# Optimization experiments

Hardware: AMD Instinct MI355X
Metric: run time of the kernel (lower is better)

Reference implementation:

```python
import jax, jax.numpy as jnp
import numpy as np

N, H, HD = 512, 8, 128          # n_nodes, n_heads, h feature dim
M0, M1 = 256, 256               # mlp_units
NORM_CONST = 1.0


def setup_inputs() -> dict:
    key = jax.random.key(0)
    ks = jax.random.split(key, 16)
    def w(k, i, o, scale=1.0):
        return jax.random.normal(k, (i, o), jnp.float32) * (scale / np.sqrt(i))
    F = HD + H * H               # h_concat dim = 128 + 64 = 192
    EIN = H + 2 * F              # edge MLP input dim = 8 + 384 = 392
    return {
        "x": jax.random.normal(ks[0], (N, H, 3), jnp.float32),
        "h": jax.random.normal(ks[1], (N, HD), jnp.float32),
        # phi_e: MLP([256,256], silu, activate_final=True)
        "We0": w(ks[2], EIN, M0), "be0": jnp.zeros((M0,), jnp.float32),
        "We1": w(ks[3], M0, M1), "be1": jnp.zeros((M1,), jnp.float32),
        # phi_inf: Linear(1) + sigmoid
        "Winf": w(ks[4], M1, 1), "binf": jnp.zeros((1,), jnp.float32),
        # phi_x: MLP([256,256], silu, activate_final=True) -> Linear(n_heads) (variance-scaled small init)
        "Wx0": w(ks[5], M1, M0), "bx0": jnp.zeros((M0,), jnp.float32),
        "Wx1": w(ks[6], M0, M1), "bx1": jnp.zeros((M1,), jnp.float32),
        "Wxo": w(ks[7], M1, H, scale=0.03), "bxo": jnp.zeros((H,), jnp.float32),
        # phi_h: MLP([256,256], silu, activate_final=False)... note haiku MLP applies
        # activation between layers; final Linear(h_dim) appended in forward.
        "Wh0": w(ks[8], M1 + HD, M0), "bh0": jnp.zeros((M0,), jnp.float32),
        "Wh1": w(ks[9], M0, M1), "bh1": jnp.zeros((M1,), jnp.float32),
        "Who": w(ks[10], M1, HD), "bho": jnp.zeros((HD,), jnp.float32),
    }


def _forward(x, h, We0, be0, We1, be1, Winf, binf, Wx0, bx0, Wx1, bx1,
             Wxo, bxo, Wh0, bh0, Wh1, bh1, Who, bho):
    n, nh = x.shape[0], x.shape[1]
    silu = jax.nn.silu
    off = 1.0 - jnp.eye(n, dtype=x.dtype)                  # off-diagonal node mask
    # per-node head-pair squared distances -> [N, H*H] (diag naturally 0)
    dh = x[:, :, None, :] - x[:, None, :, :]               # [N,H,H,3]
    sqh = jnp.sum(dh * dh, axis=-1).reshape(n, nh * nh)
    hc = jnp.concatenate([h, sqh], axis=-1)                # [N, F]
    # all-pairs node diffs per head: dn[i,j,h] = x[j,h] - x[i,h]
    dn = x[None] - x[:, None]                              # [N,N,H,3]
    sqn = jnp.sum(dn * dn, axis=-1)                        # [N,N,H]
    F = hc.shape[-1]
    hc_j = jnp.broadcast_to(hc[None], (n, n, F))           # receiver-side: hc[j]
    hc_i = jnp.broadcast_to(hc[:, None], (n, n, F))        # sender-side: hc[i]
    edge_in = jnp.concatenate([sqn, hc_j, hc_i], axis=-1)  # [N,N,H+2F]
    # phi_e (activate_final=True), zero self-edges
    m = silu(silu(edge_in @ We0 + be0) @ We1 + be1) * off[:, :, None]
    # gate + message aggregation
    e = jax.nn.sigmoid(m @ Winf + binf)[..., 0] * off      # [N,N]
    m_i = jnp.einsum('ijd,ij->id', m, e)                   # [N,M1]
    # phi_x multi-head coordinate weights (tanh=False), zero self-edges
    px = (silu(silu(m @ Wx0 + bx0) @ Wx1 + bx1) @ Wxo + bxo) * off[:, :, None]
    # normalize_by_x_norm=True path
    norm = jnp.sqrt(sqn + 1e-8) + NORM_CONST               # [N,N,H]
    ndiff = (dn / norm[..., None]) * off[:, :, None, None]
    shift = jnp.einsum('ijhd,ijh->ihd', ndiff, px) / (n - 1)  # agg='mean'
    x_new = x + shift
    # phi_h with residual
    ph_in = jnp.concatenate([m_i, h], axis=-1)
    h_new = h + silu(silu(ph_in @ Wh0 + bh0) @ Wh1 + bh1) @ Who + bho
    return x_new, h_new


def reference(x, h, We0, be0, We1, be1, Winf, binf, Wx0, bx0, Wx1, bx1,
              Wxo, bxo, Wh0, bh0, Wh1, bh1, Who, bho):
    return _forward(x, h, We0, be0, We1, be1, Winf, binf, Wx0, bx0, Wx1, bx1,
                    Wxo, bxo, Wh0, bh0, Wh1, bh1, Who, bho)
```

## Files before the change

kernel.cpp:

```cpp
#include <hip/hip_runtime.h>
#include <math.h>

#define N_NODES 512
#define NH 8
#define HD 128
#define M 256
#define JTILE 32

typedef __bf16 v8bf __attribute__((ext_vector_type(8)));
typedef float f32x4 __attribute__((ext_vector_type(4)));
typedef unsigned uint2v __attribute__((ext_vector_type(2)));

__device__ __forceinline__ float silu_f(float v) {
  return v * __builtin_amdgcn_rcpf(1.f + __expf(-v));
}
__device__ __forceinline__ float sigmoid_f(float v) {
  return __builtin_amdgcn_rcpf(1.f + __expf(-v));
}
__device__ __forceinline__ unsigned short f2bf(float f) {
  unsigned u = __float_as_uint(f);
  u += 0x7fffu + ((u >> 16) & 1u);
  return (unsigned short)(u >> 16);
}
__device__ __forceinline__ float bf2f_lo(unsigned u) {
  return __uint_as_float(u << 16);
}
__device__ __forceinline__ float bf2f_hi(unsigned u) {
  return __uint_as_float(u & 0xffff0000u);
}
__device__ __forceinline__ unsigned cvt_pk_bf16(float lo, float hi) {
  unsigned r;
  asm("v_cvt_pk_bf16_f32 %0, %1, %2" : "=v"(r) : "v"(lo), "v"(hi));
  return r;
}

__global__ __launch_bounds__(256) void k_pre(
    const float* __restrict__ x, const float* __restrict__ h,
    const float* __restrict__ We0, const float* __restrict__ be0,
    const float* __restrict__ We1, const float* __restrict__ Wx0,
    const float* __restrict__ Wx1, const float* __restrict__ Wxo,
    unsigned short* __restrict__ wsB,
    float* __restrict__ P, float* __restrict__ Q,
    float* __restrict__ mi, float* __restrict__ shift)
{
  const int t = threadIdx.x;
  if (blockIdx.x < 816) {
    const int gid = blockIdx.x * 256 + t;
    if (gid >= 208896) return;
    float val;
    int dst;
    if (gid < 196608) {
      const int layer = gid >> 16, e = gid & 65535;
      const int k = e >> 8, n = e & 255;
      const float* W = (layer == 0) ? We1 : (layer == 1) ? Wx0 : Wx1;
      val = W[e];
      const int kt = k >> 5, w = k & 31, quad = w >> 3, j = w & 7;
      const int nt = n >> 4, lnib = n & 15;
      dst = layer * 65536 + ((kt * 16 + nt) * 64 + quad * 16 + lnib) * 8 + j;
    } else if (gid < 198656) {
      const int e = gid - 196608;
      val = Wxo[e];
      const int k = e >> 3, col = e & 7;
      const int kt = k >> 5, w = k & 31, quad = w >> 3, j = w & 7;
      dst = 196608 + (kt * 64 + quad * 16 + col) * 8 + j;
    } else if (gid < 200704) {
      const int e = gid - 198656;
      val = 0.f;
      const int k = e >> 3, col = e & 7;
      const int kt = k >> 5, w = k & 31, quad = w >> 3, j = w & 7;
      dst = 196608 + (kt * 64 + quad * 16 + col + 8) * 8 + j;
    } else if (gid < 202752) {
      const int e = gid - 200704;
      val = We0[e];
      const int j = e >> 8, n = e & 255, nt = n >> 4, lnib = n & 15;
      dst = 200704 + (nt * 64 + lnib) * 8 + j;
    } else {
      const int e = gid - 202752;
      val = 0.f;
      const int q = 1 + (e >> 11), rem = e & 2047;
      const int j = rem & 7, lnib = (rem >> 3) & 15, nt = rem >> 7;
      dst = 200704 + (nt * 64 + q * 16 + lnib) * 8 + j;
    }
    wsB[dst] = f2bf(val);
    return;
  }
  const int i = blockIdx.x - 816;
  __shared__ float s_x[24];
  __shared__ float s_hc[192];
  mi[i * M + t] = 0.f;
  if (t < 24) { shift[i * 24 + t] = 0.f; s_x[t] = x[i * 24 + t]; }
  __syncthreads();
  if (t < HD) {
    s_hc[t] = h[i * HD + t];
  } else if (t < 192) {
    const int p = t - HD, a = p >> 3, b = p & 7;
    float s = 0.f;
#pragma unroll
    for (int d = 0; d < 3; ++d) {
      const float dx = s_x[a * 3 + d] - s_x[b * 3 + d];
      s = fmaf(dx, dx, s);
    }
    s_hc[t] = s;
  }
  __syncthreads();
  float p = 0.f, q = 0.f;
  for (int k = 0; k < 192; ++k) {
    const float hv = s_hc[k];
    p = fmaf(hv, We0[(8 + k) * M + t], p);
    q = fmaf(hv, We0[(200 + k) * M + t], q);
  }
  P[i * M + t] = p;
  Q[i * M + t] = q + be0[t];
}

__global__ __launch_bounds__(256, 5) void k_edge(
    const float* __restrict__ x,
    const float* __restrict__ P, const float* __restrict__ Q,
    const float* __restrict__ be1,
    const float* __restrict__ Winf, const float* __restrict__ binf,
    const float* __restrict__ bx0, const float* __restrict__ bx1,
    const float* __restrict__ bxo,
    const unsigned short* __restrict__ wsB,
    float* __restrict__ mi_acc, float* __restrict__ shift_acc)
{
  const int i  = blockIdx.x;
  const int j0 = blockIdx.y * JTILE;
  const int t  = threadIdx.x;
  const int lane = t & 63, wq = t >> 6;
  const int lnib = lane & 15, quad = lane >> 4;
  const int cb = wq * 64;

  __shared__ __align__(16) unsigned short a_act[16 * 512];
  __shared__ __align__(16) float s_sqn[JTILE][8];
  __shared__ __align__(16) unsigned short s_sqnb[JTILE][8];
  __shared__ float s_red[JTILE][4];
  __shared__ float s_e[JTILE];

  f32x4 acc[4][2];

  auto store_frag = [&](int ct, int et, unsigned w0, unsigned w1) {
    const int tile = et * 8 + 2 * wq + (ct >> 1);
    const int qp   = (ct & 1) * 2 + (quad >> 1);
    const int sidx = (tile * 64 + qp * 16 + lnib) * 8 + (quad & 1) * 4;
    *(uint2v*)&a_act[sidx] = (uint2v){w0, w1};
  };

  auto run_gemm = [&](const unsigned short* __restrict__ Bg) {
#pragma unroll
    for (int kt = 0; kt < 8; ++kt) {
      v8bf wf[4], af[2];
#pragma unroll
      for (int ct = 0; ct < 4; ++ct)
        wf[ct] = *(const v8bf*)&Bg[((kt * 16 + wq * 4 + ct) * 64 + lane) * 8];
#pragma unroll
      for (int et = 0; et < 2; ++et)
        af[et] = *(const v8bf*)&a_act[((et * 8 + kt) * 64 + lane) * 8];
#pragma unroll
      for (int ct = 0; ct < 4; ++ct)
#pragma unroll
        for (int et = 0; et < 2; ++et)
          acc[ct][et] = __builtin_amdgcn_mfma_f32_16x16x32_bf16(wf[ct], af[et], acc[ct][et], 0, 0, 0);
    }
  };

  {
    const int r = t >> 3, hh = t & 7;
    const int j = j0 + r;
    float s = 0.f;
#pragma unroll
    for (int d = 0; d < 3; ++d) {
      const float dx = x[j * 24 + hh * 3 + d] - x[i * 24 + hh * 3 + d];
      s = fmaf(dx, dx, s);
    }
    s_sqn[r][hh] = s;
    s_sqnb[r][hh] = f2bf(s);
  }
  const float binf0 = binf[0];
  __syncthreads();

  {
#pragma unroll
    for (int ct = 0; ct < 4; ++ct)
#pragma unroll
      for (int et = 0; et < 2; ++et)
        acc[ct][et] = *(const f32x4*)&P[(j0 + et * 16 + lnib) * M + cb + ct * 16 + quad * 4];
    const unsigned short* W0 = wsB + 200704;
    v8bf wf[4], af[2];
#pragma unroll
    for (int ct = 0; ct < 4; ++ct)
      wf[ct] = *(const v8bf*)&W0[((wq * 4 + ct) * 64 + lane) * 8];
#pragma unroll
    for (int et = 0; et < 2; ++et)
      af[et] = *(const v8bf*)&s_sqnb[et * 16 + lnib][0];
#pragma unroll
    for (int ct = 0; ct < 4; ++ct)
#pragma unroll
      for (int et = 0; et < 2; ++et)
        acc[ct][et] = __builtin_amdgcn_mfma_f32_16x16x32_bf16(wf[ct], af[et], acc[ct][et], 0, 0, 0);
#pragma unroll
    for (int ct = 0; ct < 4; ++ct) {
      const f32x4 qv = *(const f32x4*)&Q[i * M + cb + ct * 16 + quad * 4];
#pragma unroll
      for (int et = 0; et < 2; ++et) {
        const unsigned w0 = cvt_pk_bf16(silu_f(acc[ct][et][0] + qv[0]),
                                        silu_f(acc[ct][et][1] + qv[1]));
        const unsigned w1 = cvt_pk_bf16(silu_f(acc[ct][et][2] + qv[2]),
                                        silu_f(acc[ct][et][3] + qv[3]));
        store_frag(ct, et, w0, w1);
      }
    }
  }

#pragma unroll
  for (int ct = 0; ct < 4; ++ct) {
    const f32x4 b = *(const f32x4*)&be1[cb + ct * 16 + quad * 4];
#pragma unroll
    for (int et = 0; et < 2; ++et) acc[ct][et] = b;
  }
  __syncthreads();
  run_gemm(wsB);
  __syncthreads();

  unsigned mw[4][2][2];
  {
    float ge[2] = {0.f, 0.f};
#pragma unroll
    for (int ct = 0; ct < 4; ++ct) {
      const f32x4 wv = *(const f32x4*)&Winf[cb + ct * 16 + quad * 4];
#pragma unroll
      for (int et = 0; et < 2; ++et) {
        const int row = et * 16 + lnib;
        const bool dz = (j0 + row == i);
        const float v0 = dz ? 0.f : silu_f(acc[ct][et][0]);
        const float v1 = dz ? 0.f : silu_f(acc[ct][et][1]);
        const float v2 = dz ? 0.f : silu_f(acc[ct][et][2]);
        const float v3 = dz ? 0.f : silu_f(acc[ct][et][3]);
        ge[et] = fmaf(v0, wv[0], ge[et]);
        ge[et] = fmaf(v1, wv[1], ge[et]);
        ge[et] = fmaf(v2, wv[2], ge[et]);
        ge[et] = fmaf(v3, wv[3], ge[et]);
        const unsigned w0 = cvt_pk_bf16(v0, v1);
        const unsigned w1 = cvt_pk_bf16(v2, v3);
        mw[ct][et][0] = w0; mw[ct][et][1] = w1;
        store_frag(ct, et, w0, w1);
      }
    }
#pragma unroll
    for (int et = 0; et < 2; ++et) {
      float g = ge[et];
      g += __shfl_xor(g, 16);
      g += __shfl_xor(g, 32);
      if (quad == 0) s_red[et * 16 + lnib][wq] = g;
    }
  }
  __syncthreads();
  if (t < JTILE)
    s_e[t] = sigmoid_f(s_red[t][0] + s_red[t][1] + s_red[t][2] + s_red[t][3] + binf0);
  __syncthreads();

  {
    float ev[2];
#pragma unroll
    for (int et = 0; et < 2; ++et) ev[et] = s_e[et * 16 + lnib];
    float s[4][4];
#pragma unroll
    for (int ct = 0; ct < 4; ++ct) {
      s[ct][0] = 0.f; s[ct][1] = 0.f; s[ct][2] = 0.f; s[ct][3] = 0.f;
#pragma unroll
      for (int et = 0; et < 2; ++et) {
        s[ct][0] = fmaf(bf2f_lo(mw[ct][et][0]), ev[et], s[ct][0]);
        s[ct][1] = fmaf(bf2f_hi(mw[ct][et][0]), ev[et], s[ct][1]);
        s[ct][2] = fmaf(bf2f_lo(mw[ct][et][1]), ev[et], s[ct][2]);
        s[ct][3] = fmaf(bf2f_hi(mw[ct][et][1]), ev[et], s[ct][3]);
      }
    }
#pragma unroll
    for (int ct = 0; ct < 4; ++ct)
#pragma unroll
      for (int r = 0; r < 4; ++r) {
        float v = s[ct][r];
        v += __shfl_xor(v, 1);
        v += __shfl_xor(v, 2);
        v += __shfl_xor(v, 4);
        v += __shfl_xor(v, 8);
        s[ct][r] = v;
      }
    if (lnib == 0) {
#pragma unroll
      for (int ct = 0; ct < 4; ++ct)
#pragma unroll
        for (int r = 0; r < 4; ++r)
          atomicAdd(&mi_acc[i * M + cb + ct * 16 + quad * 4 + r], s[ct][r]);
    }
  }

#pragma unroll
  for (int ct = 0; ct < 4; ++ct) {
    const f32x4 b = *(const f32x4*)&bx0[cb + ct * 16 + quad * 4];
#pragma unroll
    for (int et = 0; et < 2; ++et) acc[ct][et] = b;
  }
  run_gemm(wsB + 65536);
  __syncthreads();
#pragma unroll
  for (int ct = 0; ct < 4; ++ct)
#pragma unroll
    for (int et = 0; et < 2; ++et) {
      const unsigned w0 = cvt_pk_bf16(silu_f(acc[ct][et][0]), silu_f(acc[ct][et][1]));
      const unsigned w1 = cvt_pk_bf16(silu_f(acc[ct][et][2]), silu_f(acc[ct][et][3]));
      store_frag(ct, et, w0, w1);
    }

#pragma unroll
  for (int ct = 0; ct < 4; ++ct) {
    const f32x4 b = *(const f32x4*)&bx1[cb + ct * 16 + quad * 4];
#pragma unroll
    for (int et = 0; et < 2; ++et) acc[ct][et] = b;
  }
  __syncthreads();
  run_gemm(wsB + 131072);
  __syncthreads();
#pragma unroll
  for (int ct = 0; ct < 4; ++ct)
#pragma unroll
    for (int et = 0; et < 2; ++et) {
      const unsigned w0 = cvt_pk_bf16(silu_f(acc[ct][et][0]), silu_f(acc[ct][et][1]));
      const unsigned w1 = cvt_pk_bf16(silu_f(acc[ct][et][2]), silu_f(acc[ct][et][3]));
      store_frag(ct, et, w0, w1);
    }
  __syncthreads();

  if (wq < 2) {
    f32x4 px;
    if (quad < 2) px = *(const f32x4*)&bxo[quad * 4];
    else          px = (f32x4){0.f, 0.f, 0.f, 0.f};
    const unsigned short* Bx = wsB + 196608;
#pragma unroll
    for (int kt = 0; kt < 8; ++kt) {
      const v8bf af = *(const v8bf*)&a_act[((wq * 8 + kt) * 64 + lane) * 8];
      const v8bf wf = *(const v8bf*)&Bx[(kt * 64 + lane) * 8];
      px = __builtin_amdgcn_mfma_f32_16x16x32_bf16(wf, af, px, 0, 0, 0);
    }
    const int e0 = wq * 16;
    const int jg = j0 + e0 + lnib;
    float c0[4], c1[4], c2[4];
#pragma unroll
    for (int r = 0; r < 4; ++r) { c0[r] = 0.f; c1[r] = 0.f; c2[r] = 0.f; }
    if (quad < 2 && jg != i) {
#pragma unroll
      for (int r = 0; r < 4; ++r) {
        const int hh = quad * 4 + r;
        const float sq = s_sqn[e0 + lnib][hh];
        const float f  = px[r] * __builtin_amdgcn_rcpf(sqrtf(sq + 1e-8f) + 1.f);
        c0[r] = (x[jg * 24 + hh * 3 + 0] - x[i * 24 + hh * 3 + 0]) * f;
        c1[r] = (x[jg * 24 + hh * 3 + 1] - x[i * 24 + hh * 3 + 1]) * f;
        c2[r] = (x[jg * 24 + hh * 3 + 2] - x[i * 24 + hh * 3 + 2]) * f;
      }
    }
#pragma unroll
    for (int r = 0; r < 4; ++r) {
#pragma unroll
      for (int s = 1; s <= 8; s <<= 1) {
        c0[r] += __shfl_xor(c0[r], s);
        c1[r] += __shfl_xor(c1[r], s);
        c2[r] += __shfl_xor(c2[r], s);
      }
    }
    if (lnib == 0 && quad < 2) {
#pragma unroll
      for (int r = 0; r < 4; ++r) {
        const int hh = quad * 4 + r;
        atomicAdd(&shift_acc[i * 24 + hh * 3 + 0], c0[r]);
        atomicAdd(&shift_acc[i * 24 + hh * 3 + 1], c1[r]);
        atomicAdd(&shift_acc[i * 24 + hh * 3 + 2], c2[r]);
      }
    }
  }
}

__global__ __launch_bounds__(256) void k_hout(
    const float* __restrict__ x, const float* __restrict__ shift,
    const float* __restrict__ h, const float* __restrict__ mi,
    const float* __restrict__ Wh0, const float* __restrict__ bh0,
    const float* __restrict__ Wh1, const float* __restrict__ bh1,
    const float* __restrict__ Who, const float* __restrict__ bho,
    float* __restrict__ out_x, float* __restrict__ out_h)
{
  const int i = blockIdx.x, t = threadIdx.x;
  __shared__ float s_in[M + HD];
  __shared__ float s_b[M];
  if (t < 24) out_x[i * 24 + t] = x[i * 24 + t] + shift[i * 24 + t] * (1.f / 511.f);
  s_in[t] = mi[i * M + t];
  if (t < HD) s_in[M + t] = h[i * HD + t];
  __syncthreads();
  float acc = bh0[t];
  for (int k = 0; k < M + HD; ++k) acc = fmaf(s_in[k], Wh0[k * M + t], acc);
  s_b[t] = silu_f(acc);
  __syncthreads();
  float acc2 = bh1[t];
  for (int k = 0; k < M; ++k) acc2 = fmaf(s_b[k], Wh1[k * M + t], acc2);
  const float a1v = silu_f(acc2);
  __syncthreads();
  s_in[t] = a1v;
  __syncthreads();
  if (t < HD) {
    float o = bho[t];
    for (int k = 0; k < M; ++k) o = fmaf(s_in[k], Who[k * HD + t], o);
    out_h[i * HD + t] = h[i * HD + t] + o;
  }
}

extern "C" void kernel_launch(void* const* d_in, const int* in_sizes, int n_in,
                              void* d_out, int out_size, void* d_ws, size_t ws_size,
                              hipStream_t stream)
{
  const float* x    = (const float*)d_in[0];
  const float* h    = (const float*)d_in[1];
  const float* We0  = (const float*)d_in[2];
  const float* be0  = (const float*)d_in[3];
  const float* We1  = (const float*)d_in[4];
  const float* be1  = (const float*)d_in[5];
  const float* Winf = (const float*)d_in[6];
  const float* binf = (const float*)d_in[7];
  const float* Wx0  = (const float*)d_in[8];
  const float* bx0  = (const float*)d_in[9];
  const float* Wx1  = (const float*)d_in[10];
  const float* bx1  = (const float*)d_in[11];
  const float* Wxo  = (const float*)d_in[12];
  const float* bxo  = (const float*)d_in[13];
  const float* Wh0  = (const float*)d_in[14];
  const float* bh0  = (const float*)d_in[15];
  const float* Wh1  = (const float*)d_in[16];
  const float* bh1  = (const float*)d_in[17];
  const float* Who  = (const float*)d_in[18];
  const float* bho  = (const float*)d_in[19];

  float* out_x = (float*)d_out;
  float* out_h = out_x + N_NODES * NH * 3;

  float* ws    = (float*)d_ws;
  float* mi    = ws;
  float* shift = ws + 131072;
  float* P     = ws + 143360;
  float* Q     = ws + 274432;
  unsigned short* wsB = (unsigned short*)(ws + 405504);

  k_pre<<<816 + N_NODES, 256, 0, stream>>>(
      x, h, We0, be0, We1, Wx0, Wx1, Wxo, wsB, P, Q, mi, shift);
  k_edge<<<dim3(N_NODES, N_NODES / JTILE), 256, 0, stream>>>(
      x, P, Q, be1, Winf, binf, bx0, bx1, bxo, wsB, mi, shift);
  k_hout<<<N_NODES, 256, 0, stream>>>(
      x, shift, h, mi, Wh0, bh0, Wh1, bh1, Who, bho, out_x, out_h);
}
```

Before: 349.2 us.

## Double edge tile to 64 rows with 512-thread blocks and prefetched GEMM fragments

Each edge block now covers 64 j-nodes with 8 waves, split into column groups and edge-row halves. The block count halves and per-block work doubles, so each weight fragment load is shared across more edge rows. The inner GEMM loop double-buffers weight and activation fragments so the next k-step loads overlap the current MFMAs. Message values for the aggregation are re-read from shared memory instead of being held in registers, which frees registers at the cost of extra LDS reads, and LDS use per block doubles.

```diff
diff --git a/kernel.cpp b/kernel.cpp
--- a/kernel.cpp
+++ b/kernel.cpp
@@ -5,7 +5,7 @@
 #define NH 8
 #define HD 128
 #define M 256
-#define JTILE 32
+#define JTILE 64
 
 typedef __bf16 v8bf __attribute__((ext_vector_type(8)));
 typedef float f32x4 __attribute__((ext_vector_type(4)));
@@ -113,7 +113,7 @@
   Q[i * M + t] = q + be0[t];
 }
 
-__global__ __launch_bounds__(256, 5) void k_edge(
+__global__ __launch_bounds__(512, 4) void k_edge(
     const float* __restrict__ x,
     const float* __restrict__ P, const float* __restrict__ Q,
     const float* __restrict__ be1,
@@ -128,9 +128,12 @@
   const int t  = threadIdx.x;
   const int lane = t & 63, wq = t >> 6;
   const int lnib = lane & 15, quad = lane >> 4;
-  const int cb = wq * 64;
-
-  __shared__ __align__(16) unsigned short a_act[16 * 512];
+  const int wqc = __builtin_amdgcn_readfirstlane(wq >> 1);
+  const int wqe = __builtin_amdgcn_readfirstlane(wq & 1);
+  const int cb = wqc * 64;
+  const int wqe2 = wqe * 2;
+
+  __shared__ __align__(16) unsigned short a_act[32 * 512];
   __shared__ __align__(16) float s_sqn[JTILE][8];
   __shared__ __align__(16) unsigned short s_sqnb[JTILE][8];
   __shared__ float s_red[JTILE][4];
@@ -138,28 +141,39 @@
 
   f32x4 acc[4][2];
 
+  auto frag_addr = [&](int ct, int et) {
+    return ((((wqe2 + et) * 8 + wqc * 2 + (ct >> 1)) * 64 +
+             ((ct & 1) * 2 + (quad >> 1)) * 16 + lnib) * 8) + (quad & 1) * 4;
+  };
   auto store_frag = [&](int ct, int et, unsigned w0, unsigned w1) {
-    const int tile = et * 8 + 2 * wq + (ct >> 1);
-    const int qp   = (ct & 1) * 2 + (quad >> 1);
-    const int sidx = (tile * 64 + qp * 16 + lnib) * 8 + (quad & 1) * 4;
-    *(uint2v*)&a_act[sidx] = (uint2v){w0, w1};
+    *(uint2v*)&a_act[frag_addr(ct, et)] = (uint2v){w0, w1};
   };
 
   auto run_gemm = [&](const unsigned short* __restrict__ Bg) {
+    const unsigned short* Bw = Bg + wqc * 2048;
+    v8bf wf[2][4], af[2][2];
+#pragma unroll
+    for (int ct = 0; ct < 4; ++ct)
+      wf[0][ct] = *(const v8bf*)&Bw[(ct * 64 + lane) * 8];
+#pragma unroll
+    for (int et = 0; et < 2; ++et)
+      af[0][et] = *(const v8bf*)&a_act[(((wqe2 + et) * 8) * 64 + lane) * 8];
 #pragma unroll
     for (int kt = 0; kt < 8; ++kt) {
-      v8bf wf[4], af[2];
+      const int cur = kt & 1, nxt = cur ^ 1;
+      if (kt < 7) {
+#pragma unroll
+        for (int ct = 0; ct < 4; ++ct)
+          wf[nxt][ct] = *(const v8bf*)&Bw[(((kt + 1) * 16 + ct) * 64 + lane) * 8];
+#pragma unroll
+        for (int et = 0; et < 2; ++et)
+          af[nxt][et] = *(const v8bf*)&a_act[(((wqe2 + et) * 8 + kt + 1) * 64 + lane) * 8];
+      }
 #pragma unroll
       for (int ct = 0; ct < 4; ++ct)
-        wf[ct] = *(const v8bf*)&Bg[((kt * 16 + wq * 4 + ct) * 64 + lane) * 8];
-#pragma unroll
-      for (int et = 0; et < 2; ++et)
-        af[et] = *(const v8bf*)&a_act[((et * 8 + kt) * 64 + lane) * 8];
-#pragma unroll
-      for (int ct = 0; ct < 4; ++ct)
 #pragma unroll
         for (int et = 0; et < 2; ++et)
-          acc[ct][et] = __builtin_amdgcn_mfma_f32_16x16x32_bf16(wf[ct], af[et], acc[ct][et], 0, 0, 0);
+          acc[ct][et] = __builtin_amdgcn_mfma_f32_16x16x32_bf16(wf[cur][ct], af[cur][et], acc[ct][et], 0, 0, 0);
     }
   };
 
@@ -183,15 +197,15 @@
     for (int ct = 0; ct < 4; ++ct)
 #pragma unroll
       for (int et = 0; et < 2; ++et)
-        acc[ct][et] = *(const f32x4*)&P[(j0 + et * 16 + lnib) * M + cb + ct * 16 + quad * 4];
-    const unsigned short* W0 = wsB + 200704;
+        acc[ct][et] = *(const f32x4*)&P[(j0 + (wqe2 + et) * 16 + lnib) * M + cb + ct * 16 + quad * 4];
+    const unsigned short* W0 = wsB + 200704 + wqc * 2048;
     v8bf wf[4], af[2];
 #pragma unroll
     for (int ct = 0; ct < 4; ++ct)
-      wf[ct] = *(const v8bf*)&W0[((wq * 4 + ct) * 64 + lane) * 8];
+      wf[ct] = *(const v8bf*)&W0[(ct * 64 + lane) * 8];
 #pragma unroll
     for (int et = 0; et < 2; ++et)
-      af[et] = *(const v8bf*)&s_sqnb[et * 16 + lnib][0];
+      af[et] = *(const v8bf*)&s_sqnb[(wqe2 + et) * 16 + lnib][0];
 #pragma unroll
     for (int ct = 0; ct < 4; ++ct)
 #pragma unroll
@@ -221,7 +235,6 @@
   run_gemm(wsB);
   __syncthreads();
 
-  unsigned mw[4][2][2];
   {
     float ge[2] = {0.f, 0.f};
 #pragma unroll
@@ -229,7 +242,7 @@
       const f32x4 wv = *(const f32x4*)&Winf[cb + ct * 16 + quad * 4];
 #pragma unroll
       for (int et = 0; et < 2; ++et) {
-        const int row = et * 16 + lnib;
+        const int row = (wqe2 + et) * 16 + lnib;
         const bool dz = (j0 + row == i);
         const float v0 = dz ? 0.f : silu_f(acc[ct][et][0]);
         const float v1 = dz ? 0.f : silu_f(acc[ct][et][1]);
@@ -239,10 +252,7 @@
         ge[et] = fmaf(v1, wv[1], ge[et]);
         ge[et] = fmaf(v2, wv[2], ge[et]);
         ge[et] = fmaf(v3, wv[3], ge[et]);
-        const unsigned w0 = cvt_pk_bf16(v0, v1);
-        const unsigned w1 = cvt_pk_bf16(v2, v3);
-        mw[ct][et][0] = w0; mw[ct][et][1] = w1;
-        store_frag(ct, et, w0, w1);
+        store_frag(ct, et, cvt_pk_bf16(v0, v1), cvt_pk_bf16(v2, v3));
       }
     }
 #pragma unroll
@@ -250,7 +260,7 @@
       float g = ge[et];
       g += __shfl_xor(g, 16);
       g += __shfl_xor(g, 32);
-      if (quad == 0) s_red[et * 16 + lnib][wq] = g;
+      if (quad == 0) s_red[(wqe2 + et) * 16 + lnib][wqc] = g;
     }
   }
   __syncthreads();
@@ -261,17 +271,18 @@
   {
     float ev[2];
 #pragma unroll
-    for (int et = 0; et < 2; ++et) ev[et] = s_e[et * 16 + lnib];
+    for (int et = 0; et < 2; ++et) ev[et] = s_e[(wqe2 + et) * 16 + lnib];
     float s[4][4];
 #pragma unroll
     for (int ct = 0; ct < 4; ++ct) {
       s[ct][0] = 0.f; s[ct][1] = 0.f; s[ct][2] = 0.f; s[ct][3] = 0.f;
 #pragma unroll
       for (int et = 0; et < 2; ++et) {
-        s[ct][0] = fmaf(bf2f_lo(mw[ct][et][0]), ev[et], s[ct][0]);
-        s[ct][1] = fmaf(bf2f_hi(mw[ct][et][0]), ev[et], s[ct][1]);
-        s[ct][2] = fmaf(bf2f_lo(mw[ct][et][1]), ev[et], s[ct][2]);
-        s[ct][3] = fmaf(bf2f_hi(mw[ct][et][1]), ev[et], s[ct][3]);
+        const uint2v pw = *(const uint2v*)&a_act[frag_addr(ct, et)];
+        s[ct][0] = fmaf(bf2f_lo(pw[0]), ev[et], s[ct][0]);
+        s[ct][1] = fmaf(bf2f_hi(pw[0]), ev[et], s[ct][1]);
+        s[ct][2] = fmaf(bf2f_lo(pw[1]), ev[et], s[ct][2]);
+        s[ct][3] = fmaf(bf2f_hi(pw[1]), ev[et], s[ct][3]);
       }
     }
 #pragma unroll
@@ -330,7 +341,7 @@
     }
   __syncthreads();
 
-  if (wq < 2) {
+  if (wq < 4) {
     f32x4 px;
     if (quad < 2) px = *(const f32x4*)&bxo[quad * 4];
     else          px = (f32x4){0.f, 0.f, 0.f, 0.f};
@@ -447,7 +458,7 @@
 
   k_pre<<<816 + N_NODES, 256, 0, stream>>>(
       x, h, We0, be0, We1, Wx0, Wx1, Wxo, wsB, P, Q, mi, shift);
-  k_edge<<<dim3(N_NODES, N_NODES / JTILE), 256, 0, stream>>>(
+  k_edge<<<dim3(N_NODES, N_NODES / JTILE), 512, 0, stream>>>(
       x, P, Q, be1, Winf, binf, bx0, bx1, bxo, wsB, mi, shift);
   k_hout<<<N_NODES, 256, 0, stream>>>(
       x, shift, h, mi, Wh0, bh0, Wh1, bh1, Who, bho, out_x, out_h);
```

Result: no change. 343.3 us (-1.7%).
